# Performance work log

Measured on AMD Instinct MI355X. Metric: run time of the kernel, lower is better.

## Reference

```python
import jax, jax.numpy as jnp
import numpy as np

B, T, C, H = 2, 2048, 1024, 16
D = C // H  # head_dim = 64

def setup_inputs() -> dict:
    key = jax.random.key(0)
    k1, k2, k3, k4, k5 = jax.random.split(key, 5)
    x = jax.random.normal(k1, (B, T, C), dtype=jnp.float32)
    # RoPE tables (realistic frequencies)
    inv_freq = 1.0 / (10000.0 ** (jnp.arange(0, D // 2, dtype=jnp.float32) / (D // 2)))
    pos = jnp.arange(T, dtype=jnp.float32)
    ang = pos[:, None] * inv_freq[None, :]          # (T, D/2)
    cos, sin = jnp.cos(ang), jnp.sin(ang)
    # causal mask (True = keep)
    mask = jnp.tril(jnp.ones((T, T), dtype=bool))
    W_qkv = jax.random.normal(k2, (3 * C, C), dtype=jnp.float32) * (1.0 / np.sqrt(C))
    W_out = jax.random.normal(k3, (C, C), dtype=jnp.float32) * (1.0 / np.sqrt(C))
    return {"x": x, "cos": cos, "sin": sin, "mask": mask, "W_qkv": W_qkv, "W_out": W_out}

def apply_rope(x, cos, sin):
    # x: (B, H, T, D); cos/sin: (T, D/2)
    d = x.shape[-1] // 2
    x1, x2 = x[..., :d], x[..., d:]
    c = cos[None, None, :x.shape[2], :]
    s = sin[None, None, :x.shape[2], :]
    return jnp.concatenate([x1 * c - x2 * s, x2 * c + x1 * s], axis=-1)

def reference(x, cos, sin, mask, W_qkv, W_out):
    b, t, c = x.shape
    qkv = (x @ W_qkv.T).reshape(b, t, 3, H, D)
    q, k, v = qkv[:, :, 0], qkv[:, :, 1], qkv[:, :, 2]   # (b, t, H, D)
    q = q.transpose(0, 2, 1, 3)
    k = k.transpose(0, 2, 1, 3)
    v = v.transpose(0, 2, 1, 3)                           # (b, H, t, D)
    q = apply_rope(q, cos, sin)
    k = apply_rope(k, cos, sin)
    attn = jnp.einsum('bhqd,bhkd->bhqk', q, k) / jnp.sqrt(jnp.asarray(D, x.dtype))
    attn = jnp.where(mask[None, None, :, :], attn, -jnp.inf)
    attn = jax.nn.softmax(attn, axis=-1)
    out = jnp.einsum('bhqk,bhkd->bhqd', attn, v)          # (b, H, t, D)
    out = out.transpose(0, 2, 1, 3).reshape(b, t, c)
    return out @ W_out.T
```

## Files before the change

### kernel.cpp

```cpp
#include <hip/hip_runtime.h>
#include <stdint.h>

typedef __bf16 bf16;
typedef __bf16 bf16x4 __attribute__((ext_vector_type(4)));
typedef __bf16 bf16x8 __attribute__((ext_vector_type(8)));
typedef float f32x4 __attribute__((ext_vector_type(4)));

#define TSEQ 2048
#define NHEAD 16
#define HDIM 64
#define CDIM 1024

#define AS1(p) ((const __attribute__((address_space(1))) void*)(p))
#define AS3(p) ((__attribute__((address_space(3))) void*)(p))

#if __has_builtin(__builtin_amdgcn_exp2f)
#define EXP2(x) __builtin_amdgcn_exp2f(x)
#else
#define EXP2(x) exp2f(x)
#endif

__global__ __launch_bounds__(256) void cast3_bf16(const float* __restrict__ in1, int n1,
                                                  const float* __restrict__ in2, int n2,
                                                  const float* __restrict__ in3, int n3,
                                                  bf16* __restrict__ out1,
                                                  bf16* __restrict__ out2,
                                                  bf16* __restrict__ out3) {
  int i = (blockIdx.x * 256 + threadIdx.x) * 8;
  const float* src;
  bf16* dst;
  if (i < n1) {
    src = in1 + i; dst = out1 + i;
  } else if (i < n1 + n2) {
    src = in2 + (i - n1); dst = out2 + (i - n1);
  } else if (i < n1 + n2 + n3) {
    src = in3 + (i - n1 - n2); dst = out3 + (i - n1 - n2);
  } else {
    return;
  }
  float4 a = *(const float4*)src;
  float4 b = *(const float4*)(src + 4);
  bf16x8 r;
  r[0] = (bf16)a.x; r[1] = (bf16)a.y; r[2] = (bf16)a.z; r[3] = (bf16)a.w;
  r[4] = (bf16)b.x; r[5] = (bf16)b.y; r[6] = (bf16)b.z; r[7] = (bf16)b.w;
  *(bf16x8*)dst = r;
}

__global__ __launch_bounds__(256) void gemm_qkv_rope(const bf16* __restrict__ A,
                                                     const bf16* __restrict__ B,
                                                     const float* __restrict__ cosb,
                                                     const float* __restrict__ sinb,
                                                     bf16* __restrict__ Qb,
                                                     bf16* __restrict__ Kb,
                                                     bf16* __restrict__ Vt) {
  constexpr int K = 1024;
  __shared__ bf16 smem[8704];
  const int t = threadIdx.x;
  const int w = t >> 6, l = t & 63, g = l >> 4, ln = l & 15;
  const int wm = (w >> 1) * 64, wn = (w & 1) * 64;
  const int m0 = blockIdx.x * 128, n0 = blockIdx.y * 128;
  const int r0 = t >> 2, kc0 = (t & 3) * 8;

  f32x4 acc[4][4] = {};

  for (int k0 = 0; k0 < K; k0 += 32) {
    __syncthreads();
    __builtin_amdgcn_global_load_lds(AS1(A + (size_t)(m0 + r0) * K + k0 + kc0),
                                     AS3(&smem[t * 8]), 16, 0, 0);
    __builtin_amdgcn_global_load_lds(AS1(A + (size_t)(m0 + r0 + 64) * K + k0 + kc0),
                                     AS3(&smem[(t + 256) * 8]), 16, 0, 0);
    __builtin_amdgcn_global_load_lds(AS1(B + (size_t)(n0 + r0) * K + k0 + kc0),
                                     AS3(&smem[4096 + t * 8]), 16, 0, 0);
    __builtin_amdgcn_global_load_lds(AS1(B + (size_t)(n0 + r0 + 64) * K + k0 + kc0),
                                     AS3(&smem[4096 + (t + 256) * 8]), 16, 0, 0);
    __syncthreads();
    bf16x8 af[4], bfr[4];
#pragma unroll
    for (int i = 0; i < 4; i++) {
      af[i] = *(const bf16x8*)&smem[(wm + i * 16 + ln) * 32 + g * 8];
      bfr[i] = *(const bf16x8*)&smem[4096 + (wn + i * 16 + ln) * 32 + g * 8];
    }
#pragma unroll
    for (int i = 0; i < 4; i++)
#pragma unroll
      for (int j = 0; j < 4; j++)
        acc[i][j] = __builtin_amdgcn_mfma_f32_16x16x32_bf16(af[i], bfr[j], acc[i][j], 0, 0, 0);
  }

  const int part = n0 >> 10;
  if (part < 2) {
    bf16* dst = part ? Kb : Qb;
    const float qs = part ? 1.0f : 0.18033688011112042f;
#pragma unroll
    for (int i = 0; i < 4; i++)
#pragma unroll
      for (int j = 0; j < 2; j++) {
        int nl = (n0 & 1023) + wn + j * 16 + ln;
        int h = nl >> 6, d = nl & 31;
#pragma unroll
        for (int r = 0; r < 4; r++) {
          int row = m0 + wm + i * 16 + g * 4 + r;
          int tok = row & (TSEQ - 1), bb = row >> 11;
          float c = cosb[tok * 32 + d], s = sinb[tok * 32 + d];
          float a1 = acc[i][j][r], a2 = acc[i][j + 2][r];
          size_t ob = ((size_t)(bb * NHEAD + h) * TSEQ + tok) * HDIM + d;
          dst[ob] = (bf16)((a1 * c - a2 * s) * qs);
          dst[ob + 32] = (bf16)((a2 * c + a1 * s) * qs);
        }
      }
  } else {
    const int bb = m0 >> 11;
    const int tbase = m0 & (TSEQ - 1);
    const int nbase = n0 - 2048;
#pragma unroll
    for (int pass = 0; pass < 2; pass++) {
      __syncthreads();
      if ((w >> 1) == pass) {
#pragma unroll
        for (int i = 0; i < 4; i++)
#pragma unroll
          for (int j = 0; j < 4; j++) {
            int lr = i * 16 + g * 4;
            int lc = wn + j * 16 + ln;
#pragma unroll
            for (int r = 0; r < 4; r++)
              smem[(lr + r) * 132 + lc] = (bf16)acc[i][j][r];
          }
      }
      __syncthreads();
      for (int c = t; c < 1024; c += 256) {
        int ch = c >> 3, tc = c & 7;
        bf16x8 o;
#pragma unroll
        for (int j2 = 0; j2 < 8; j2++) o[j2] = smem[(tc * 8 + j2) * 132 + ch];
        int n = nbase + ch;
        int h = n >> 6, d = n & 63;
        *(bf16x8*)(Vt + ((size_t)((bb * NHEAD + h) * HDIM + d)) * TSEQ +
                   tbase + pass * 64 + tc * 8) = o;
      }
    }
  }
}

__global__ __launch_bounds__(256) void gemm_out(const bf16* __restrict__ A,
                                                const bf16* __restrict__ B,
                                                float* __restrict__ C,
                                                int M, int N, int K) {
  __shared__ bf16 As[64 * 32];
  __shared__ bf16 Bs[128 * 32];
  const int t = threadIdx.x;
  const int w = t >> 6, l = t & 63, g = l >> 4, ln = l & 15;
  const int m0 = blockIdx.x * 64, n0 = blockIdx.y * 128;
  const int r0 = t >> 2, kc0 = (t & 3) * 8;

  f32x4 acc[4][2] = {};

  for (int k0 = 0; k0 < K; k0 += 32) {
    __syncthreads();
    __builtin_amdgcn_global_load_lds(AS1(A + (size_t)(m0 + r0) * K + k0 + kc0),
                                     AS3(&As[t * 8]), 16, 0, 0);
    __builtin_amdgcn_global_load_lds(AS1(B + (size_t)(n0 + r0) * K + k0 + kc0),
                                     AS3(&Bs[t * 8]), 16, 0, 0);
    __builtin_amdgcn_global_load_lds(AS1(B + (size_t)(n0 + r0 + 64) * K + k0 + kc0),
                                     AS3(&Bs[(t + 256) * 8]), 16, 0, 0);
    __syncthreads();
    bf16x8 af[4], bfr[2];
#pragma unroll
    for (int i = 0; i < 4; i++)
      af[i] = *(const bf16x8*)&As[(i * 16 + ln) * 32 + g * 8];
#pragma unroll
    for (int j = 0; j < 2; j++)
      bfr[j] = *(const bf16x8*)&Bs[(w * 32 + j * 16 + ln) * 32 + g * 8];
#pragma unroll
    for (int i = 0; i < 4; i++)
#pragma unroll
      for (int j = 0; j < 2; j++)
        acc[i][j] = __builtin_amdgcn_mfma_f32_16x16x32_bf16(af[i], bfr[j], acc[i][j], 0, 0, 0);
  }
#pragma unroll
  for (int i = 0; i < 4; i++)
#pragma unroll
    for (int j = 0; j < 2; j++) {
      int row = m0 + i * 16 + g * 4;
      int col = n0 + w * 32 + j * 16 + ln;
#pragma unroll
      for (int r = 0; r < 4; r++)
        C[(size_t)(row + r) * N + col] = acc[i][j][r];
    }
}

__global__ __launch_bounds__(256) void attn_fwd(const bf16* __restrict__ Q,
                                                const bf16* __restrict__ K,
                                                const bf16* __restrict__ Vt,
                                                bf16* __restrict__ ctx) {
  __shared__ bf16 Ks[64 * 72];
  __shared__ bf16 VTs[64 * 72];
  __shared__ bf16 Ps[4][16 * 72];

  const int t = threadIdx.x;
  const int w = t >> 6;
  const int l = t & 63, g = l >> 4, ln = l & 15;
  const int bid = blockIdx.x;
  const int bh = bid & 31;
  const int qb = 31 - (bid >> 5);
  const size_t base = (size_t)bh * TSEQ * HDIM;

  const int r0 = t >> 3, ch0 = (t & 7) * 8;
  const int q0 = qb * 64;
  const int q_global = q0 + w * 16 + ln;
  const int px = (ln & 8) ? 32 : 0;

  bf16x8 bq[2];
  bq[0] = *(const bf16x8*)(Q + base + (size_t)q_global * HDIM + g * 8);
  bq[1] = *(const bf16x8*)(Q + base + (size_t)q_global * HDIM + 32 + g * 8);

  const bf16* kp0 = K + base + (size_t)r0 * HDIM + ch0;
  const bf16* kp1 = K + base + (size_t)(r0 + 32) * HDIM + ch0;
  const bf16* vp0 = Vt + base + (size_t)r0 * TSEQ + ch0;
  const bf16* vp1 = Vt + base + (size_t)(r0 + 32) * TSEQ + ch0;

  bf16x8 kr0 = *(const bf16x8*)kp0;
  bf16x8 kr1 = *(const bf16x8*)kp1;
  bf16x8 vr0 = *(const bf16x8*)vp0;
  bf16x8 vr1 = *(const bf16x8*)vp1;

  f32x4 acc[4] = {};
  float l_run = 0.f;

  for (int kt = 0; kt <= qb; kt++) {
    __syncthreads();
    *(bf16x8*)&Ks[r0 * 72 + ch0] = kr0;
    *(bf16x8*)&Ks[(r0 + 32) * 72 + ch0] = kr1;
    *(bf16x8*)&VTs[r0 * 72 + ch0] = vr0;
    *(bf16x8*)&VTs[(r0 + 32) * 72 + ch0] = vr1;
    __syncthreads();
    if (kt < qb) {
      kr0 = *(const bf16x8*)(kp0 + (kt + 1) * 64 * HDIM);
      kr1 = *(const bf16x8*)(kp1 + (kt + 1) * 64 * HDIM);
      vr0 = *(const bf16x8*)(vp0 + (kt + 1) * 64);
      vr1 = *(const bf16x8*)(vp1 + (kt + 1) * 64);
    }

    f32x4 st[4] = {};
#pragma unroll
    for (int step = 0; step < 2; step++)
#pragma unroll
      for (int mt = 0; mt < 4; mt++) {
        bf16x8 ak = *(const bf16x8*)&Ks[(mt * 16 + ln) * 72 + step * 32 + g * 8];
        st[mt] = __builtin_amdgcn_mfma_f32_16x16x32_bf16(ak, bq[step], st[mt], 0, 0, 0);
      }
    float vals[16];
    if (kt == qb) {
#pragma unroll
      for (int mt = 0; mt < 4; mt++)
#pragma unroll
        for (int r = 0; r < 4; r++) {
          int kg = kt * 64 + mt * 16 + g * 4 + r;
          vals[mt * 4 + r] = (kg <= q_global) ? fminf(st[mt][r], 60.f) : -INFINITY;
        }
    } else {
#pragma unroll
      for (int mt = 0; mt < 4; mt++)
#pragma unroll
        for (int r = 0; r < 4; r++) vals[mt * 4 + r] = fminf(st[mt][r], 60.f);
    }
    float psum = 0.f;
#pragma unroll
    for (int i2 = 0; i2 < 16; i2++) {
      float p = EXP2(vals[i2]);
      vals[i2] = p;
      psum += p;
    }
    psum += __shfl_xor(psum, 16);
    psum += __shfl_xor(psum, 32);
    l_run += psum;
#pragma unroll
    for (int mt = 0; mt < 4; mt++) {
      bf16x4 pk;
#pragma unroll
      for (int r = 0; r < 4; r++) pk[r] = (bf16)vals[mt * 4 + r];
      *(bf16x4*)&Ps[w][ln * 72 + ((mt * 16 + g * 4) ^ px)] = pk;
    }
#pragma unroll
    for (int step = 0; step < 2; step++) {
      bf16x8 ap = *(const bf16x8*)&Ps[w][ln * 72 + ((step * 32 + g * 8) ^ px)];
#pragma unroll
      for (int nt = 0; nt < 4; nt++) {
        bf16x8 bv = *(const bf16x8*)&VTs[(nt * 16 + ln) * 72 + step * 32 + g * 8];
        acc[nt] = __builtin_amdgcn_mfma_f32_16x16x32_bf16(ap, bv, acc[nt], 0, 0, 0);
      }
    }
  }

  float inv = 1.0f / l_run;
  float lrow[4];
#pragma unroll
  for (int r = 0; r < 4; r++) lrow[r] = __shfl(inv, g * 4 + r, 64);
  const int b = bh >> 4, h = bh & (NHEAD - 1);
#pragma unroll
  for (int nt = 0; nt < 4; nt++)
#pragma unroll
    for (int r = 0; r < 4; r++) {
      int q = q0 + w * 16 + g * 4 + r;
      ctx[(size_t)(b * TSEQ + q) * CDIM + h * HDIM + nt * 16 + ln] =
          (bf16)(acc[nt][r] * lrow[r]);
    }
}

extern "C" void kernel_launch(void* const* d_in, const int* in_sizes, int n_in,
                              void* d_out, int out_size, void* d_ws, size_t ws_size,
                              hipStream_t stream) {
  const float* x = (const float*)d_in[0];
  const float* cosb = (const float*)d_in[1];
  const float* sinb = (const float*)d_in[2];
  const float* Wqkv = (const float*)d_in[4];
  const float* Wout = (const float*)d_in[5];
  float* out = (float*)d_out;

  char* ws = (char*)d_ws;
  bf16* x_bf = (bf16*)ws;
  bf16* ctx = (bf16*)ws;
  bf16* Wqkv_bf = (bf16*)(ws + 8388608);
  bf16* Wout_bf = (bf16*)(ws + 14680064);
  bf16* Qb = (bf16*)(ws + 16777216);
  bf16* Kb = (bf16*)(ws + 25165824);
  bf16* Vt = (bf16*)(ws + 33554432);

  cast3_bf16<<<(4194304 + 3145728 + 1048576) / 8 / 256, 256, 0, stream>>>(
      x, 4194304, Wqkv, 3145728, Wout, 1048576, x_bf, Wqkv_bf, Wout_bf);
  gemm_qkv_rope<<<dim3(32, 24), 256, 0, stream>>>(x_bf, Wqkv_bf, cosb, sinb, Qb, Kb, Vt);
  attn_fwd<<<1024, 256, 0, stream>>>(Qb, Kb, Vt, ctx);
  gemm_out<<<dim3(64, 8), 256, 0, stream>>>(ctx, Wout_bf, out, 4096, 1024, 1024);
}
```

Before: 191.0 us.

## Use 128-query attention blocks with XOR-swizzled LDS and MFMA priority hints

Result: faster. 184.8 us (-3.3%).

```diff
diff --git a/kernel.cpp b/kernel.cpp
--- a/kernel.cpp
+++ b/kernel.cpp
@@ -189,106 +189,107 @@
     }
 }
 
-__global__ __launch_bounds__(256) void attn_fwd(const bf16* __restrict__ Q,
+__global__ __launch_bounds__(512) void attn_fwd(const bf16* __restrict__ Q,
                                                 const bf16* __restrict__ K,
                                                 const bf16* __restrict__ Vt,
                                                 bf16* __restrict__ ctx) {
-  __shared__ bf16 Ks[64 * 72];
-  __shared__ bf16 VTs[64 * 72];
-  __shared__ bf16 Ps[4][16 * 72];
+  __shared__ bf16 Ks[64 * 64];
+  __shared__ bf16 VTs[64 * 64];
+  __shared__ bf16 Ps[8][16 * 64];
 
   const int t = threadIdx.x;
   const int w = t >> 6;
   const int l = t & 63, g = l >> 4, ln = l & 15;
   const int bid = blockIdx.x;
   const int bh = bid & 31;
-  const int qb = 31 - (bid >> 5);
+  const int qb0 = 15 - (bid >> 5);
   const size_t base = (size_t)bh * TSEQ * HDIM;
 
+  const int q0 = qb0 * 128;
+  const int qwb = q0 + w * 16;
+  const int dtile = qwb >> 6;
+  const int ktmax = 2 * qb0 + 1;
+  const int q_global = qwb + ln;
+  const int lswz = (ln & 7) * 8;
+
   const int r0 = t >> 3, ch0 = (t & 7) * 8;
-  const int q0 = qb * 64;
-  const int q_global = q0 + w * 16 + ln;
-  const int px = (ln & 8) ? 32 : 0;
+  const int sidx = r0 * 64 + (((t & 7) ^ (r0 & 7)) * 8);
 
   bf16x8 bq[2];
   bq[0] = *(const bf16x8*)(Q + base + (size_t)q_global * HDIM + g * 8);
   bq[1] = *(const bf16x8*)(Q + base + (size_t)q_global * HDIM + 32 + g * 8);
 
-  const bf16* kp0 = K + base + (size_t)r0 * HDIM + ch0;
-  const bf16* kp1 = K + base + (size_t)(r0 + 32) * HDIM + ch0;
-  const bf16* vp0 = Vt + base + (size_t)r0 * TSEQ + ch0;
-  const bf16* vp1 = Vt + base + (size_t)(r0 + 32) * TSEQ + ch0;
-
-  bf16x8 kr0 = *(const bf16x8*)kp0;
-  bf16x8 kr1 = *(const bf16x8*)kp1;
-  bf16x8 vr0 = *(const bf16x8*)vp0;
-  bf16x8 vr1 = *(const bf16x8*)vp1;
+  const bf16* kp = K + base + (size_t)r0 * HDIM + ch0;
+  const bf16* vp = Vt + base + (size_t)r0 * TSEQ + ch0;
+  bf16x8 kr = *(const bf16x8*)kp;
+  bf16x8 vr = *(const bf16x8*)vp;
 
   f32x4 acc[4] = {};
   float l_run = 0.f;
 
-  for (int kt = 0; kt <= qb; kt++) {
-    __syncthreads();
-    *(bf16x8*)&Ks[r0 * 72 + ch0] = kr0;
-    *(bf16x8*)&Ks[(r0 + 32) * 72 + ch0] = kr1;
-    *(bf16x8*)&VTs[r0 * 72 + ch0] = vr0;
-    *(bf16x8*)&VTs[(r0 + 32) * 72 + ch0] = vr1;
-    __syncthreads();
-    if (kt < qb) {
-      kr0 = *(const bf16x8*)(kp0 + (kt + 1) * 64 * HDIM);
-      kr1 = *(const bf16x8*)(kp1 + (kt + 1) * 64 * HDIM);
-      vr0 = *(const bf16x8*)(vp0 + (kt + 1) * 64);
-      vr1 = *(const bf16x8*)(vp1 + (kt + 1) * 64);
-    }
-
-    f32x4 st[4] = {};
-#pragma unroll
-    for (int step = 0; step < 2; step++)
+  for (int kt = 0; kt <= ktmax; kt++) {
+    __syncthreads();
+    *(bf16x8*)&Ks[sidx] = kr;
+    *(bf16x8*)&VTs[sidx] = vr;
+    __syncthreads();
+    if (kt < ktmax) {
+      kr = *(const bf16x8*)(kp + (size_t)(kt + 1) * 64 * HDIM);
+      vr = *(const bf16x8*)(vp + (kt + 1) * 64);
+    }
+    if (kt <= dtile) {
+      f32x4 st[4] = {};
+      __builtin_amdgcn_s_setprio(1);
+#pragma unroll
+      for (int step = 0; step < 2; step++)
+#pragma unroll
+        for (int mt = 0; mt < 4; mt++) {
+          bf16x8 ak = *(const bf16x8*)&Ks[(mt * 16 + ln) * 64 + ((step * 32 + g * 8) ^ lswz)];
+          st[mt] = __builtin_amdgcn_mfma_f32_16x16x32_bf16(ak, bq[step], st[mt], 0, 0, 0);
+        }
+      __builtin_amdgcn_s_setprio(0);
+      float vals[16];
+      if (kt == dtile) {
+#pragma unroll
+        for (int mt = 0; mt < 4; mt++)
+#pragma unroll
+          for (int r = 0; r < 4; r++) {
+            int kg = kt * 64 + mt * 16 + g * 4 + r;
+            vals[mt * 4 + r] = (kg <= q_global) ? fminf(st[mt][r], 60.f) : -INFINITY;
+          }
+      } else {
+#pragma unroll
+        for (int mt = 0; mt < 4; mt++)
+#pragma unroll
+          for (int r = 0; r < 4; r++) vals[mt * 4 + r] = fminf(st[mt][r], 60.f);
+      }
+      float psum = 0.f;
+#pragma unroll
+      for (int i2 = 0; i2 < 16; i2++) {
+        float p = EXP2(vals[i2]);
+        vals[i2] = p;
+        psum += p;
+      }
+      psum += __shfl_xor(psum, 16);
+      psum += __shfl_xor(psum, 32);
+      l_run += psum;
 #pragma unroll
       for (int mt = 0; mt < 4; mt++) {
-        bf16x8 ak = *(const bf16x8*)&Ks[(mt * 16 + ln) * 72 + step * 32 + g * 8];
-        st[mt] = __builtin_amdgcn_mfma_f32_16x16x32_bf16(ak, bq[step], st[mt], 0, 0, 0);
-      }
-    float vals[16];
-    if (kt == qb) {
-#pragma unroll
-      for (int mt = 0; mt < 4; mt++)
-#pragma unroll
-        for (int r = 0; r < 4; r++) {
-          int kg = kt * 64 + mt * 16 + g * 4 + r;
-          vals[mt * 4 + r] = (kg <= q_global) ? fminf(st[mt][r], 60.f) : -INFINITY;
+        bf16x4 pk;
+#pragma unroll
+        for (int r = 0; r < 4; r++) pk[r] = (bf16)vals[mt * 4 + r];
+        *(bf16x4*)&Ps[w][ln * 64 + (((mt * 16 + (g >> 1) * 8) ^ lswz) + (g & 1) * 4)] = pk;
+      }
+      __builtin_amdgcn_s_setprio(1);
+#pragma unroll
+      for (int step = 0; step < 2; step++) {
+        bf16x8 ap = *(const bf16x8*)&Ps[w][ln * 64 + ((step * 32 + g * 8) ^ lswz)];
+#pragma unroll
+        for (int nt = 0; nt < 4; nt++) {
+          bf16x8 bv = *(const bf16x8*)&VTs[(nt * 16 + ln) * 64 + ((step * 32 + g * 8) ^ lswz)];
+          acc[nt] = __builtin_amdgcn_mfma_f32_16x16x32_bf16(ap, bv, acc[nt], 0, 0, 0);
         }
-    } else {
-#pragma unroll
-      for (int mt = 0; mt < 4; mt++)
-#pragma unroll
-        for (int r = 0; r < 4; r++) vals[mt * 4 + r] = fminf(st[mt][r], 60.f);
-    }
-    float psum = 0.f;
-#pragma unroll
-    for (int i2 = 0; i2 < 16; i2++) {
-      float p = EXP2(vals[i2]);
-      vals[i2] = p;
-      psum += p;
-    }
-    psum += __shfl_xor(psum, 16);
-    psum += __shfl_xor(psum, 32);
-    l_run += psum;
-#pragma unroll
-    for (int mt = 0; mt < 4; mt++) {
-      bf16x4 pk;
-#pragma unroll
-      for (int r = 0; r < 4; r++) pk[r] = (bf16)vals[mt * 4 + r];
-      *(bf16x4*)&Ps[w][ln * 72 + ((mt * 16 + g * 4) ^ px)] = pk;
-    }
-#pragma unroll
-    for (int step = 0; step < 2; step++) {
-      bf16x8 ap = *(const bf16x8*)&Ps[w][ln * 72 + ((step * 32 + g * 8) ^ px)];
-#pragma unroll
-      for (int nt = 0; nt < 4; nt++) {
-        bf16x8 bv = *(const bf16x8*)&VTs[(nt * 16 + ln) * 72 + step * 32 + g * 8];
-        acc[nt] = __builtin_amdgcn_mfma_f32_16x16x32_bf16(ap, bv, acc[nt], 0, 0, 0);
-      }
+      }
+      __builtin_amdgcn_s_setprio(0);
     }
   }
 
@@ -301,7 +302,7 @@
   for (int nt = 0; nt < 4; nt++)
 #pragma unroll
     for (int r = 0; r < 4; r++) {
-      int q = q0 + w * 16 + g * 4 + r;
+      int q = qwb + g * 4 + r;
       ctx[(size_t)(b * TSEQ + q) * CDIM + h * HDIM + nt * 16 + ln] =
           (bf16)(acc[nt][r] * lrow[r]);
     }
@@ -329,6 +330,6 @@
   cast3_bf16<<<(4194304 + 3145728 + 1048576) / 8 / 256, 256, 0, stream>>>(
       x, 4194304, Wqkv, 3145728, Wout, 1048576, x_bf, Wqkv_bf, Wout_bf);
   gemm_qkv_rope<<<dim3(32, 24), 256, 0, stream>>>(x_bf, Wqkv_bf, cosb, sinb, Qb, Kb, Vt);
-  attn_fwd<<<1024, 256, 0, stream>>>(Qb, Kb, Vt, ctx);
+  attn_fwd<<<512, 512, 0, stream>>>(Qb, Kb, Vt, ctx);
   gemm_out<<<dim3(64, 8), 256, 0, stream>>>(ctx, Wout_bf, out, 4096, 1024, 1024);
 }
```
